# Kernel tuning notes

Measured on AMD Instinct MI355X. Metric: run time of the kernel, lower is better.

## Reference

```python
import jax, jax.numpy as jnp
import numpy as np

N = 100000   # nodes
E = 1600000  # edges
IN = 64
HID = 64
C = 2
EPS = 1e-12


def _linear_init(k, fan_in, fan_out):
    s = 1.0 / np.sqrt(fan_in)
    kw, kb = jax.random.split(k)
    w = jax.random.uniform(kw, (fan_in, fan_out), minval=-s, maxval=s, dtype=jnp.float32)
    b = jax.random.uniform(kb, (fan_out,), minval=-s, maxval=s, dtype=jnp.float32)
    return w, b


def setup_inputs() -> dict:
    key = jax.random.key(0)
    ks = jax.random.split(key, 12)
    x = jax.random.normal(ks[0], (N, IN), dtype=jnp.float32)
    edge_index = jax.random.randint(ks[1], (2, E), 0, N, dtype=jnp.int64)
    w1, b1 = _linear_init(ks[2], IN, HID)
    w2, b2 = _linear_init(ks[3], HID, HID)
    w3, b3 = _linear_init(ks[4], HID, HID)
    wg1, bg1 = _linear_init(ks[5], HID, HID)   # GCNConv 1
    wg2, bg2 = _linear_init(ks[6], HID, HID)   # GCNConv 2
    beta = jnp.ones((), dtype=jnp.float32)     # AGNN learnable scalar
    wf, bf = _linear_init(ks[7], HID, HID)     # W_f
    wx, bx = _linear_init(ks[8], HID, HID)     # W_x
    wc, bc = _linear_init(ks[9], 2 * HID, C)   # classifier
    return {"x": x, "edge_index": edge_index,
            "w1": w1, "b1": b1, "w2": w2, "b2": b2, "w3": w3, "b3": b3,
            "wg1": wg1, "bg1": bg1, "wg2": wg2, "bg2": bg2, "beta": beta,
            "wf": wf, "bf": bf, "wx": wx, "bx": bx, "wc": wc, "bc": bc}


def _segment_softmax(logits, seg, n):
    m = jax.ops.segment_max(logits, seg, num_segments=n)
    e = jnp.exp(logits - m[seg])
    s = jax.ops.segment_sum(e, seg, num_segments=n)
    return e / s[seg]


def _gcn_conv(x, w, b, row, col, norm):
    # x' = D^{-1/2}(A+I)D^{-1/2} x W + b  (PyG GCNConv with self-loops)
    h = x @ w                                   # [N, HID]
    msg = h[row] * norm[:, None]                # gather + scale  [E+N, HID]
    out = jax.ops.segment_sum(msg, col, num_segments=N)
    return out + b


def _agnn_conv(x, beta, row, col):
    # cosine-similarity attention (PyG AGNNConv), self-loops included
    xn = x / (jnp.linalg.norm(x, axis=-1, keepdims=True) + EPS)
    alpha = beta * jnp.sum(xn[row] * xn[col], axis=-1)   # [E+N]
    a = _segment_softmax(alpha, col, N)
    return jax.ops.segment_sum(a[:, None] * x[row], col, num_segments=N)


def reference(x, edge_index, w1, b1, w2, b2, w3, b3, wg1, bg1, wg2, bg2,
              beta, wf, bf, wx, bx, wc, bc):
    # add self-loops
    loop = jnp.arange(N, dtype=edge_index.dtype)
    row = jnp.concatenate([edge_index[0], loop])
    col = jnp.concatenate([edge_index[1], loop])
    # symmetric GCN normalization
    deg = jax.ops.segment_sum(jnp.ones_like(col, dtype=jnp.float32), col, num_segments=N)
    dinv = jnp.where(deg > 0, deg ** -0.5, 0.0)
    norm = dinv[row] * dinv[col]

    # input MLP
    h = jax.nn.relu(x @ w1 + b1)
    h = jax.nn.relu(h @ w2 + b2)
    h = h @ w3 + b3                              # [N, HID]

    f0 = _gcn_conv(h, wg1, bg1, row, col, norm)
    f1 = _gcn_conv(h, wg2, bg2, row, col, norm)
    h1 = _agnn_conv(h, beta, row, col)

    h_filters = jnp.stack([f0, f1], axis=1)      # [N, 2, HID]
    h_proj = jnp.tanh(h_filters @ wf + bf)       # [N, 2, HID]
    x_proj = jnp.tanh(h @ wx + bx)               # [N, HID]
    logit = jnp.einsum('nkh,nh->nk', h_proj, x_proj)   # bmm -> [N, 2]
    score = jax.nn.softmax(logit, axis=1)
    res = jnp.einsum('nkh,nk->nh', h_filters, score)   # attention-weighted fusion
    res = jnp.concatenate([res, h1], axis=1)     # [N, 2*HID]
    y_hat = res @ wc + bc                        # dropout disabled (eval)
    return y_hat
```

## Files before the change

### kernel.cpp

```cpp
#include <hip/hip_runtime.h>
#include <math.h>


#define SCT 8192

typedef float v2f __attribute__((ext_vector_type(2)));

__device__ __forceinline__ v2f v2fma(v2f a, v2f b, v2f c) {
#if __has_builtin(__builtin_elementwise_fma)
    return __builtin_elementwise_fma(a, b, c);
#else
    v2f r; r.x = fmaf(a.x, b.x, c.x); r.y = fmaf(a.y, b.y, c.y); return r;
#endif
}

__device__ __forceinline__ float fast_tanh(float x) {
    x = fminf(fmaxf(x, -15.f), 15.f);
    float e = __expf(2.f * x);
    return (e - 1.f) * __frcp_rn(e + 1.f);
}

__device__ __forceinline__ void fma4(float (&acc)[4], float a, const float4& w) {
    acc[0] = fmaf(a, w.x, acc[0]);
    acc[1] = fmaf(a, w.y, acc[1]);
    acc[2] = fmaf(a, w.z, acc[2]);
    acc[3] = fmaf(a, w.w, acc[3]);
}

__device__ __forceinline__ void load_rows32(const float* __restrict__ src, int row0, int n,
                                            float (*dst)[68], int t)
{
    int e = t * 8;
    int r = e >> 6, i = e & 63;
    int grow = row0 + r;
    float4 v0 = make_float4(0.f, 0.f, 0.f, 0.f), v1 = v0;
    if (grow < n) {
        const float* p = src + (size_t)grow * 64 + i;
        v0 = *(const float4*)p;
        v1 = *(const float4*)(p + 4);
    }
    *(float4*)&dst[r][i]     = v0;
    *(float4*)&dst[r][i + 4] = v1;
}

__device__ __forceinline__ void gemm_core(const float (*in)[68], const float* w,
                                          const float* b, int rg, int cg,
                                          float (&acc0)[4], float (&acc1)[4])
{
#pragma unroll
    for (int dc = 0; dc < 4; dc++) { float bb = b[4*cg + dc]; acc0[dc] = bb; acc1[dc] = bb; }
    const int r0 = 2 * rg, r1 = 2 * rg + 1;
#pragma unroll
    for (int i = 0; i < 64; i += 4) {
        float4 a0 = *(const float4*)&in[r0][i];
        float4 a1 = *(const float4*)&in[r1][i];
        float4 q0 = *(const float4*)&w[(i + 0) * 64 + 4 * cg];
        float4 q1 = *(const float4*)&w[(i + 1) * 64 + 4 * cg];
        float4 q2 = *(const float4*)&w[(i + 2) * 64 + 4 * cg];
        float4 q3 = *(const float4*)&w[(i + 3) * 64 + 4 * cg];
        fma4(acc0, a0.x, q0); fma4(acc0, a0.y, q1); fma4(acc0, a0.z, q2); fma4(acc0, a0.w, q3);
        fma4(acc1, a1.x, q0); fma4(acc1, a1.y, q1); fma4(acc1, a1.z, q2); fma4(acc1, a1.w, q3);
    }
}

__device__ __forceinline__ void gemm_core_gw(const float (*in)[68], const float* __restrict__ w,
                                             const float* b, int rg, int cg,
                                             float (&acc0)[4], float (&acc1)[4])
{
#pragma unroll
    for (int dc = 0; dc < 4; dc++) { float bb = b[4*cg + dc]; acc0[dc] = bb; acc1[dc] = bb; }
    const int r0 = 2 * rg, r1 = 2 * rg + 1;
    const float* wp = w + 4 * cg;
#pragma unroll 2
    for (int i = 0; i < 64; i += 4) {
        float4 a0 = *(const float4*)&in[r0][i];
        float4 a1 = *(const float4*)&in[r1][i];
        float4 q0 = *(const float4*)&wp[(size_t)(i + 0) * 64];
        float4 q1 = *(const float4*)&wp[(size_t)(i + 1) * 64];
        float4 q2 = *(const float4*)&wp[(size_t)(i + 2) * 64];
        float4 q3 = *(const float4*)&wp[(size_t)(i + 3) * 64];
        fma4(acc0, a0.x, q0); fma4(acc0, a0.y, q1); fma4(acc0, a0.z, q2); fma4(acc0, a0.w, q3);
        fma4(acc1, a1.x, q0); fma4(acc1, a1.y, q1); fma4(acc1, a1.z, q2); fma4(acc1, a1.w, q3);
    }
}

template <int MODE>
__device__ __forceinline__ void gemm_gw_lds(const float (*in)[68], const float* __restrict__ w,
                                            const float* b, float (*out)[68],
                                            int rg, int cg)
{
    float a0[4], a1[4];
    gemm_core_gw(in, w, b, rg, cg, a0, a1);
#pragma unroll
    for (int dc = 0; dc < 4; dc++) {
        float v0 = a0[dc], v1 = a1[dc];
        if (MODE == 1) { v0 = fmaxf(v0, 0.f); v1 = fmaxf(v1, 0.f); }
        a0[dc] = v0; a1[dc] = v1;
    }
    *(float4*)&out[2 * rg][4 * cg]     = make_float4(a0[0], a0[1], a0[2], a0[3]);
    *(float4*)&out[2 * rg + 1][4 * cg] = make_float4(a1[0], a1[1], a1[2], a1[3]);
}


__global__ __launch_bounds__(256) void k_zero(int* __restrict__ arr, int n1)
{
    int i = blockIdx.x * 256 + threadIdx.x;
    if (i < n1) arr[i] = 0;
}

__global__ __launch_bounds__(256) void k_bhist(const int* __restrict__ col,
                                               int* __restrict__ bhist, int e)
{
    __shared__ int hist[256];
    int t = threadIdx.x;
    hist[t] = 0;
    __syncthreads();
    int base = blockIdx.x * SCT;
    int end = min(e, base + SCT);
    for (int i = base + t; i < end; i += 256)
        atomicAdd(&hist[col[i] >> 9], 1);
    __syncthreads();
    if (hist[t]) atomicAdd(&bhist[t], hist[t]);
}

__global__ __launch_bounds__(256) void k_bscan(const int* __restrict__ bhist,
                                               int* __restrict__ bbase, int* __restrict__ bcur)
{
    __shared__ int s[256];
    int t = threadIdx.x;
    int v = bhist[t];
    s[t] = v;
    __syncthreads();
    for (int d = 1; d < 256; d <<= 1) {
        int u = (t >= d) ? s[t - d] : 0;
        __syncthreads();
        s[t] += u;
        __syncthreads();
    }
    int b = s[t] - v;
    bbase[t] = b;
    bcur[t] = b;
}

__global__ __launch_bounds__(256) void k_bscatter2(const int* __restrict__ row,
    const int* __restrict__ col, int* __restrict__ bcur,
    int2* __restrict__ pairs, int e, int nbk)
{
    __shared__ int hist[256], lcur[256], gb[256], s[256];
    __shared__ int2 buf[SCT];
    int t = threadIdx.x;
    int base = blockIdx.x * SCT;
    int end = min(e, base + SCT);
    hist[t] = 0;
    __syncthreads();
    for (int i = base + t; i < end; i += 256)
        atomicAdd(&hist[col[i] >> 9], 1);
    __syncthreads();
    int v = hist[t];
    s[t] = v;
    __syncthreads();
    for (int d = 1; d < 256; d <<= 1) {
        int u = (t >= d) ? s[t - d] : 0;
        __syncthreads();
        s[t] += u;
        __syncthreads();
    }
    lcur[t] = s[t] - v;
    __syncthreads();
    for (int i = base + t; i < end; i += 256) {
        int c = col[i];
        int slot = atomicAdd(&lcur[c >> 9], 1);
        buf[slot] = make_int2(row[i], c);
    }
    if (v > 0) gb[t] = atomicAdd(&bcur[t], v);
    __syncthreads();
    for (int b = 0; b < nbk; b++) {
        int cnt = hist[b];
        if (cnt == 0) continue;
        int lo = s[b] - cnt;
        int go = gb[b];
        for (int j = t; j < cnt; j += 256)
            pairs[go + j] = buf[lo + j];
    }
}

__global__ __launch_bounds__(256) void k_fill3(const int2* __restrict__ pairs,
    const int* __restrict__ bbase, const int* __restrict__ bhist,
    int* __restrict__ arr, int* __restrict__ csr, int n)
{
    __shared__ int nh[512], nc[512], s[256];
    int b = blockIdx.x, t = threadIdx.x;
    int pbase = bbase[b];
    int cnt = bhist[b];
    int nodebase = b << 9;
    nh[t] = 0; nh[t + 256] = 0;
    __syncthreads();
    for (int i = t; i < cnt; i += 256)
        atomicAdd(&nh[pairs[pbase + i].y - nodebase], 1);
    __syncthreads();
    int v0 = nh[2 * t], v1 = nh[2 * t + 1];
    int sum = v0 + v1;
    s[t] = sum;
    __syncthreads();
    for (int d = 1; d < 256; d <<= 1) {
        int u = (t >= d) ? s[t - d] : 0;
        __syncthreads();
        s[t] += u;
        __syncthreads();
    }
    int excl = s[t] - sum;
    int n0 = nodebase + 2 * t, n1 = n0 + 1;
    nc[2 * t]     = pbase + excl;
    nc[2 * t + 1] = pbase + excl + v0;
    if (n0 < n) arr[n0] = pbase + excl + v0;
    if (n1 < n) arr[n1] = pbase + excl + v0 + v1;
    __syncthreads();
    for (int i = t; i < cnt; i += 256) {
        int2 pr = pairs[pbase + i];
        int p = atomicAdd(&nc[pr.y - nodebase], 1);
        csr[p] = pr.x;
    }
}


__global__ __launch_bounds__(256) void k_pre(
    const float* __restrict__ wg1, const float* __restrict__ bg1,
    const float* __restrict__ wg2, const float* __restrict__ bg2,
    const float* __restrict__ wf,  const float* __restrict__ bf,
    const float* __restrict__ wc,  float* __restrict__ pre)
{
    __shared__ float wfs[4096];
    __shared__ float wcs[128];
    int t = threadIdx.x;
    for (int i = t; i < 4096; i += 256) wfs[i] = wf[i];
    if (t < 128) wcs[t] = wc[t];
    __syncthreads();
    int i = t & 63, jb = (t >> 6) * 16;
    float acc0[16], acc1[16];
#pragma unroll
    for (int j = 0; j < 16; j++) { acc0[j] = 0.f; acc1[j] = 0.f; }
#pragma unroll 1
    for (int k = 0; k < 64; k++) {
        float a = wg1[i * 64 + k];
        float b = wg2[i * 64 + k];
#pragma unroll
        for (int j = 0; j < 16; j++) {
            float w = wfs[k * 64 + jb + j];
            acc0[j] = fmaf(a, w, acc0[j]);
            acc1[j] = fmaf(b, w, acc1[j]);
        }
    }
#pragma unroll
    for (int j = 0; j < 16; j++) {
        pre[i * 64 + jb + j]        = acc0[j];
        pre[4096 + i * 64 + jb + j] = acc1[j];
    }
    if (t < 64) {
        float s0 = bf[t], s1 = bf[t];
#pragma unroll 1
        for (int m = 0; m < 64; m++) {
            s0 = fmaf(bg1[m], wfs[m * 64 + t], s0);
            s1 = fmaf(bg2[m], wfs[m * 64 + t], s1);
        }
        pre[8192 + t] = s0;
        pre[8256 + t] = s1;
        float u00 = 0.f, u01 = 0.f, u10 = 0.f, u11 = 0.f;
#pragma unroll 1
        for (int m = 0; m < 64; m++) {
            float g1 = wg1[t * 64 + m], g2 = wg2[t * 64 + m];
            u00 = fmaf(g1, wcs[m * 2 + 0], u00);
            u01 = fmaf(g1, wcs[m * 2 + 1], u01);
            u10 = fmaf(g2, wcs[m * 2 + 0], u10);
            u11 = fmaf(g2, wcs[m * 2 + 1], u11);
        }
        pre[8320 + t * 2]     = u00;
        pre[8320 + t * 2 + 1] = u01;
        pre[8448 + t * 2]     = u10;
        pre[8448 + t * 2 + 1] = u11;
    }
    if (t == 0) {
        float v00 = 0.f, v01 = 0.f, v10 = 0.f, v11 = 0.f;
#pragma unroll 1
        for (int m = 0; m < 64; m++) {
            v00 = fmaf(bg1[m], wcs[m * 2 + 0], v00);
            v01 = fmaf(bg1[m], wcs[m * 2 + 1], v01);
            v10 = fmaf(bg2[m], wcs[m * 2 + 0], v10);
            v11 = fmaf(bg2[m], wcs[m * 2 + 1], v11);
        }
        pre[8576] = v00; pre[8577] = v01; pre[8578] = v10; pre[8579] = v11;
    }
}


__global__ __launch_bounds__(256) void k_mlp(const float* __restrict__ x,
    const float* __restrict__ w1, const float* __restrict__ b1,
    const float* __restrict__ w2, const float* __restrict__ b2,
    const float* __restrict__ w3, const float* __restrict__ b3,
    const int* __restrict__ arr, float* __restrict__ h,
    float2* __restrict__ nrm2, int n)
{
    __shared__ float b1s[64], b2s[64], b3s[64];
    __shared__ float xs[32][68], hs[32][68];
    int t = threadIdx.x;
    if (t < 64) { b1s[t] = b1[t]; b2s[t] = b2[t]; b3s[t] = b3[t]; }
    __syncthreads();
    int cg = t & 15, rg = t >> 4;
    for (int row0 = blockIdx.x * 32; row0 < n; row0 += gridDim.x * 32) {
        load_rows32(x, row0, n, xs, t);
        __syncthreads();
        gemm_gw_lds<1>(xs, w1, b1s, hs, rg, cg);
        __syncthreads();
        gemm_gw_lds<1>(hs, w2, b2s, xs, rg, cg);
        __syncthreads();
        {
            float a0[4], a1[4];
            gemm_core_gw(xs, w3, b3s, rg, cg, a0, a1);
            int r0 = row0 + 2 * rg, r1 = r0 + 1;
            if (r0 < n) *(float4*)&h[(size_t)r0 * 64 + 4 * cg] = make_float4(a0[0], a0[1], a0[2], a0[3]);
            if (r1 < n) *(float4*)&h[(size_t)r1 * 64 + 4 * cg] = make_float4(a1[0], a1[1], a1[2], a1[3]);
            float s0 = a0[0]*a0[0] + a0[1]*a0[1] + a0[2]*a0[2] + a0[3]*a0[3];
            float s1 = a1[0]*a1[0] + a1[1]*a1[1] + a1[2]*a1[2] + a1[3]*a1[3];
#pragma unroll
            for (int d = 1; d < 16; d <<= 1) { s0 += __shfl_xor(s0, d, 64); s1 += __shfl_xor(s1, d, 64); }
            if (cg == 0) {
                if (r0 < n) {
                    int st = (r0 == 0) ? 0 : arr[r0 - 1];
                    nrm2[r0] = make_float2(1.0f / (sqrtf(s0) + 1e-12f),
                                           rsqrtf((float)(arr[r0] - st + 1)));
                }
                if (r1 < n) {
                    int st = arr[r1 - 1];
                    nrm2[r1] = make_float2(1.0f / (sqrtf(s1) + 1e-12f),
                                           rsqrtf((float)(arr[r1] - st + 1)));
                }
            }
        }
        __syncthreads();
    }
}


__global__ __launch_bounds__(256) void k_gather(const float* __restrict__ h,
    const int* __restrict__ arr, const int* __restrict__ csr,
    const float2* __restrict__ nrm2, const float* __restrict__ beta_p,
    const float* __restrict__ wc,
    float* __restrict__ agg, float2* __restrict__ yp, int n)
{
    __shared__ float reda[4][8][64];
    __shared__ float redn[4][8][64];
    int wv = threadIdx.x >> 6;
    int node = blockIdx.x * 4 + wv;
    if (node >= n) return;
    int lane = threadIdx.x & 63;
    int g = lane >> 3, s = lane & 7;
    float beta = beta_p[0];
    const char* hb = (const char*)h;

    unsigned selfoff = ((unsigned)node << 8) + ((unsigned)s << 5);
    float4 hA = *(const float4*)(hb + selfoff);
    float4 hB = *(const float4*)(hb + selfoff + 16);
    v2f hc0 = {hA.x, hA.y}, hc1 = {hA.z, hA.w};
    v2f hc2 = {hB.x, hB.y}, hc3 = {hB.z, hB.w};

    v2f sv = hc0 * hc0;
    sv = v2fma(hc1, hc1, sv); sv = v2fma(hc2, hc2, sv); sv = v2fma(hc3, hc3, sv);
    float ss = sv.x + sv.y;
#pragma unroll
    for (int d = 1; d < 8; d <<= 1) ss += __shfl_xor(ss, d, 64);
    float2 ncv = nrm2[node];
    float rnc = ncv.x, dc = ncv.y;
    float brn = beta * rnc;
    float wself = __expf(brn * ss * rnc);

    v2f a0 = {0.f,0.f}, a1 = {0.f,0.f}, a2 = {0.f,0.f}, a3 = {0.f,0.f};
    v2f n0 = {0.f,0.f}, n1 = {0.f,0.f}, n2 = {0.f,0.f}, n3 = {0.f,0.f};
    float denom = 0.f;
    if (g == 0) {
        v2f dcv = {dc, dc}, wsv = {wself, wself};
        a0 = dcv * hc0; a1 = dcv * hc1; a2 = dcv * hc2; a3 = dcv * hc3;
        n0 = wsv * hc0; n1 = wsv * hc1; n2 = wsv * hc2; n3 = wsv * hc3;
        denom = wself;
    }

    int start = (node == 0) ? 0 : arr[node - 1];
    int end = arr[node];
#pragma unroll 1
    for (int k0 = start; k0 < end; k0 += 64) {
        int m = min(64, end - k0);
        int idx = 0; float rv = 0.f, dv = 0.f;
        if (lane < m) {
            idx = csr[k0 + lane];
            float2 nd = nrm2[idx];
            rv = nd.x; dv = nd.y;
        }
        int ei = __shfl(idx, g, 64);
        unsigned eoff = ((unsigned)ei << 8) + ((unsigned)s << 5);
        float4 cA = *(const float4*)(hb + eoff);
        float4 cB = *(const float4*)(hb + eoff + 16);
#pragma unroll 1
        for (int k = 0; k < m; k += 8) {
            float4 fA = cA, fB = cB;
            if (k + 8 < m) {
                int e2 = __shfl(idx, k + 8 + g, 64);
                unsigned off2 = ((unsigned)e2 << 8) + ((unsigned)s << 5);
                cA = *(const float4*)(hb + off2);
                cB = *(const float4*)(hb + off2 + 16);
            }
            float rnr = __shfl(rv, k + g, 64);
            float dvr = __shfl(dv, k + g, 64);
            v2f f0 = {fA.x, fA.y}, f1 = {fA.z, fA.w};
            v2f f2 = {fB.x, fB.y}, f3 = {fB.z, fB.w};
            v2f ps = f0 * hc0;
            ps = v2fma(f1, hc1, ps); ps = v2fma(f2, hc2, ps); ps = v2fma(f3, hc3, ps);
            float p = ps.x + ps.y;
#pragma unroll
            for (int d = 1; d < 8; d <<= 1) p += __shfl_xor(p, d, 64);
            bool act = (k + g) < m;
            float w   = act ? __expf(brn * p * rnr) : 0.f;
            float dve = act ? dvr : 0.f;
            v2f wsp = {w, w}, dsp = {dve, dve};
            a0 = v2fma(dsp, f0, a0); a1 = v2fma(dsp, f1, a1);
            a2 = v2fma(dsp, f2, a2); a3 = v2fma(dsp, f3, a3);
            n0 = v2fma(wsp, f0, n0); n1 = v2fma(wsp, f1, n1);
            n2 = v2fma(wsp, f2, n2); n3 = v2fma(wsp, f3, n3);
            denom += w;
        }
    }

    {
        float* wa = &reda[wv][g][8 * s];
        float* wn = &redn[wv][g][8 * s];
        *(float4*)wa       = make_float4(a0.x, a0.y, a1.x, a1.y);
        *(float4*)(wa + 4) = make_float4(a2.x, a2.y, a3.x, a3.y);
        *(float4*)wn       = make_float4(n0.x, n0.y, n1.x, n1.y);
        *(float4*)(wn + 4) = make_float4(n2.x, n2.y, n3.x, n3.y);
    }
    const float* ra = &reda[wv][0][lane];
    const float* rn = &redn[wv][0][lane];
    float asum, nsum;
    {
        float t0 = ra[0]   + ra[64],  t1 = ra[128] + ra[192];
        float t2 = ra[256] + ra[320], t3 = ra[384] + ra[448];
        asum = (t0 + t1) + (t2 + t3);
        float u0 = rn[0]   + rn[64],  u1 = rn[128] + rn[192];
        float u2 = rn[256] + rn[320], u3 = rn[384] + rn[448];
        nsum = (u0 + u1) + (u2 + u3);
    }
    agg[(size_t)node * 64 + lane] = dc * asum;

#pragma unroll
    for (int d = 8; d < 64; d <<= 1) denom += __shfl_xor(denom, d, 64);

    float2 wcv = *(const float2*)(wc + 128 + 2 * lane);
    float cx = nsum * wcv.x, cy = nsum * wcv.y;
#pragma unroll
    for (int d = 1; d < 64; d <<= 1) { cx += __shfl_xor(cx, d, 64); cy += __shfl_xor(cy, d, 64); }
    if (lane == 0) {
        float inv = 1.0f / denom;
        yp[node] = make_float2(cx * inv, cy * inv);
    }
}


__global__ __launch_bounds__(256) void k_epi(const float* __restrict__ agg,
    const float* __restrict__ hbuf, const float2* __restrict__ yp,
    const float* __restrict__ pre, const float* __restrict__ wx,
    const float* __restrict__ bx, const float* __restrict__ bc,
    float* __restrict__ y, int n, int ntiles)
{
    __shared__ float W0s[4096], W1s[4096], wxs[4096];
    __shared__ float c0s[64], c1s[64], bxs[64], us[256], vs[4], bcs[2];
    __shared__ float A[32][68], H[32][68];
    int t = threadIdx.x;
    for (int i = t; i < 4096; i += 256) { W0s[i] = pre[i]; W1s[i] = pre[4096 + i]; wxs[i] = wx[i]; }
    if (t < 64) { c0s[t] = pre[8192 + t]; c1s[t] = pre[8256 + t]; bxs[t] = bx[t]; }
    us[t] = pre[8320 + t];
    if (t < 4) vs[t] = pre[8576 + t];
    if (t < 2) bcs[t] = bc[t];
    __syncthreads();
    int cg = t & 15, rg = t >> 4;
    for (int tile = blockIdx.x; tile < ntiles; tile += gridDim.x) {
        int row0 = tile * 32;
        load_rows32(agg,  row0, n, A, t);
        load_rows32(hbuf, row0, n, H, t);
        __syncthreads();
        int r0g = row0 + 2 * rg, r1g = r0g + 1;
        float xp0[4], xp1[4];
        gemm_core(H, wxs, bxs, rg, cg, xp0, xp1);
#pragma unroll
        for (int j = 0; j < 4; j++) { xp0[j] = fast_tanh(xp0[j]); xp1[j] = fast_tanh(xp1[j]); }
        float a0[4], a1[4];
        gemm_core(A, W0s, c0s, rg, cg, a0, a1);
        float l00 = 0.f, l01 = 0.f;
#pragma unroll
        for (int j = 0; j < 4; j++) {
            l00 = fmaf(fast_tanh(a0[j]), xp0[j], l00);
            l01 = fmaf(fast_tanh(a1[j]), xp1[j], l01);
        }
        gemm_core(A, W1s, c1s, rg, cg, a0, a1);
        float l10 = 0.f, l11 = 0.f;
#pragma unroll
        for (int j = 0; j < 4; j++) {
            l10 = fmaf(fast_tanh(a0[j]), xp0[j], l10);
            l11 = fmaf(fast_tanh(a1[j]), xp1[j], l11);
        }
        float4 av0 = *(const float4*)&A[2 * rg][4 * cg];
        float4 av1 = *(const float4*)&A[2 * rg + 1][4 * cg];
        float za0=0.f, za1=0.f, zb0=0.f, zb1=0.f;
        float zc0=0.f, zc1=0.f, zd0=0.f, zd1=0.f;
#pragma unroll
        for (int j = 0; j < 4; j++) {
            int k = 4 * cg + j;
            float u0c0 = us[k * 2], u0c1 = us[k * 2 + 1];
            float u1c0 = us[128 + k * 2], u1c1 = us[128 + k * 2 + 1];
            float p0 = (&av0.x)[j], p1 = (&av1.x)[j];
            za0 = fmaf(p0, u0c0, za0); za1 = fmaf(p0, u0c1, za1);
            zb0 = fmaf(p0, u1c0, zb0); zb1 = fmaf(p0, u1c1, zb1);
            zc0 = fmaf(p1, u0c0, zc0); zc1 = fmaf(p1, u0c1, zc1);
            zd0 = fmaf(p1, u1c0, zd0); zd1 = fmaf(p1, u1c1, zd1);
        }
#pragma unroll
        for (int d = 1; d < 16; d <<= 1) {
            l00 += __shfl_xor(l00, d, 64); l01 += __shfl_xor(l01, d, 64);
            l10 += __shfl_xor(l10, d, 64); l11 += __shfl_xor(l11, d, 64);
            za0 += __shfl_xor(za0, d, 64); za1 += __shfl_xor(za1, d, 64);
            zb0 += __shfl_xor(zb0, d, 64); zb1 += __shfl_xor(zb1, d, 64);
            zc0 += __shfl_xor(zc0, d, 64); zc1 += __shfl_xor(zc1, d, 64);
            zd0 += __shfl_xor(zd0, d, 64); zd1 += __shfl_xor(zd1, d, 64);
        }
        if (cg == 0) {
            if (r0g < n) {
                float mx = fmaxf(l00, l10);
                float e0 = __expf(l00 - mx), e1 = __expf(l10 - mx);
                float inv = 1.0f / (e0 + e1);
                float s0 = e0 * inv, s1 = e1 * inv;
                float2 ypv = yp[r0g];
                float y0v = s0 * (za0 + vs[0]) + s1 * (zb0 + vs[2]) + ypv.x + bcs[0];
                float y1v = s0 * (za1 + vs[1]) + s1 * (zb1 + vs[3]) + ypv.y + bcs[1];
                *(float2*)&y[(size_t)r0g * 2] = make_float2(y0v, y1v);
            }
            if (r1g < n) {
                float mx = fmaxf(l01, l11);
                float e0 = __expf(l01 - mx), e1 = __expf(l11 - mx);
                float inv = 1.0f / (e0 + e1);
                float s0 = e0 * inv, s1 = e1 * inv;
                float2 ypv = yp[r1g];
                float y0v = s0 * (zc0 + vs[0]) + s1 * (zd0 + vs[2]) + ypv.x + bcs[0];
                float y1v = s0 * (zc1 + vs[1]) + s1 * (zd1 + vs[3]) + ypv.y + bcs[1];
                *(float2*)&y[(size_t)r1g * 2] = make_float2(y0v, y1v);
            }
        }
        __syncthreads();
    }
}

extern "C" void kernel_launch(void* const* d_in, const int* in_sizes, int n_in,
                              void* d_out, int out_size, void* d_ws, size_t ws_size,
                              hipStream_t stream)
{
    const float* x    = (const float*)d_in[0];
    const int*   ei   = (const int*)d_in[1];
    const float* w1   = (const float*)d_in[2];
    const float* b1   = (const float*)d_in[3];
    const float* w2   = (const float*)d_in[4];
    const float* b2   = (const float*)d_in[5];
    const float* w3   = (const float*)d_in[6];
    const float* b3   = (const float*)d_in[7];
    const float* wg1  = (const float*)d_in[8];
    const float* bg1  = (const float*)d_in[9];
    const float* wg2  = (const float*)d_in[10];
    const float* bg2  = (const float*)d_in[11];
    const float* beta = (const float*)d_in[12];
    const float* wf   = (const float*)d_in[13];
    const float* bf   = (const float*)d_in[14];
    const float* wx   = (const float*)d_in[15];
    const float* bx   = (const float*)d_in[16];
    const float* wc   = (const float*)d_in[17];
    const float* bc   = (const float*)d_in[18];
    float* y = (float*)d_out;

    int n = in_sizes[0] / 64;
    int e = in_sizes[1] / 2;
    const int* row = ei;
    const int* col = ei + e;

    char* p = (char*)d_ws;
    auto alloc = [&](size_t bytes) { char* q = p; p += (bytes + 255) & ~(size_t)255; return q; };
    float*  h    = (float*)alloc((size_t)n * 64 * 4);
    int*    csr  = (int*)alloc((size_t)e * 4);
    float2* nrm2 = (float2*)alloc((size_t)n * 8);
    int*    arr  = (int*)alloc((size_t)(n + 1) * 4);
    float2* yp   = (float2*)alloc((size_t)n * 8);
    float*  pre  = (float*)alloc(8704 * 4);
    int*    bhist = (int*)alloc(256 * 4);
    int*    bbase = (int*)alloc(256 * 4);
    int*    bcur  = (int*)alloc(256 * 4);

    int2* pairs = (int2*)h;
    float* agg = (float*)d_in[0];

    int ntiles = (n + 31) / 32;
    int nbk = (n + 511) >> 9;
    int nsct = (e + SCT - 1) / SCT;

    k_pre<<<1, 256, 0, stream>>>(wg1, bg1, wg2, bg2, wf, bf, wc, pre);
    k_zero<<<1, 256, 0, stream>>>(bhist, 256);
    k_bhist<<<nsct, 256, 0, stream>>>(col, bhist, e);
    k_bscan<<<1, 256, 0, stream>>>(bhist, bbase, bcur);
    k_bscatter2<<<nsct, 256, 0, stream>>>(row, col, bcur, pairs, e, nbk);
    k_fill3<<<nbk, 256, 0, stream>>>(pairs, bbase, bhist, arr, csr, n);
    k_mlp<<<ntiles, 256, 0, stream>>>(x, w1, b1, w2, b2, w3, b3, arr, h, nrm2, n);
    k_gather<<<(n + 3) / 4, 256, 0, stream>>>(h, arr, csr, nrm2, beta, wc, agg, yp, n);
    k_epi<<<1024, 256, 0, stream>>>(agg, h, yp, pre, wx, bx, bc, y, n, ntiles);
}
```

Measured before the change: 428.3 us.

## Make MLP per-wave with 4 rows per thread and no block barriers

The input MLP kernel now gives each wavefront a private 16-row LDS tile. Each thread computes 4 rows by 4 columns, so every global weight load is reused across four rows instead of two. The block-wide __syncthreads are replaced with wave-local LDS waitcnt fences, and blocks now cover 64 rows. This is meant to halve weight-fetch traffic per output and remove block barrier stalls. The cost is more accumulator registers, and correctness relies on the wave executing in lockstep over its own LDS region.

```diff
diff --git a/kernel.cpp b/kernel.cpp
--- a/kernel.cpp
+++ b/kernel.cpp
@@ -12,6 +12,10 @@
 #else
     v2f r; r.x = fmaf(a.x, b.x, c.x); r.y = fmaf(a.y, b.y, c.y); return r;
 #endif
+}
+
+__device__ __forceinline__ void lds_fence() {
+    asm volatile("s_waitcnt lgkmcnt(0)" ::: "memory");
 }
 
 __device__ __forceinline__ float fast_tanh(float x) {
@@ -63,42 +67,30 @@
     }
 }
 
-__device__ __forceinline__ void gemm_core_gw(const float (*in)[68], const float* __restrict__ w,
-                                             const float* b, int rg, int cg,
-                                             float (&acc0)[4], float (&acc1)[4])
-{
-#pragma unroll
-    for (int dc = 0; dc < 4; dc++) { float bb = b[4*cg + dc]; acc0[dc] = bb; acc1[dc] = bb; }
-    const int r0 = 2 * rg, r1 = 2 * rg + 1;
+__device__ __forceinline__ void gemm4_gw(const float (*in)[68], const float* __restrict__ w,
+                                         const float* b, int rgs, int cg,
+                                         float (&acc)[4][4])
+{
+#pragma unroll
+    for (int r = 0; r < 4; r++) {
+#pragma unroll
+        for (int dc = 0; dc < 4; dc++) acc[r][dc] = b[4 * cg + dc];
+    }
     const float* wp = w + 4 * cg;
+    const int r0 = 4 * rgs;
 #pragma unroll 2
     for (int i = 0; i < 64; i += 4) {
-        float4 a0 = *(const float4*)&in[r0][i];
-        float4 a1 = *(const float4*)&in[r1][i];
-        float4 q0 = *(const float4*)&wp[(size_t)(i + 0) * 64];
-        float4 q1 = *(const float4*)&wp[(size_t)(i + 1) * 64];
-        float4 q2 = *(const float4*)&wp[(size_t)(i + 2) * 64];
-        float4 q3 = *(const float4*)&wp[(size_t)(i + 3) * 64];
-        fma4(acc0, a0.x, q0); fma4(acc0, a0.y, q1); fma4(acc0, a0.z, q2); fma4(acc0, a0.w, q3);
-        fma4(acc1, a1.x, q0); fma4(acc1, a1.y, q1); fma4(acc1, a1.z, q2); fma4(acc1, a1.w, q3);
-    }
-}
-
-template <int MODE>
-__device__ __forceinline__ void gemm_gw_lds(const float (*in)[68], const float* __restrict__ w,
-                                            const float* b, float (*out)[68],
-                                            int rg, int cg)
-{
-    float a0[4], a1[4];
-    gemm_core_gw(in, w, b, rg, cg, a0, a1);
-#pragma unroll
-    for (int dc = 0; dc < 4; dc++) {
-        float v0 = a0[dc], v1 = a1[dc];
-        if (MODE == 1) { v0 = fmaxf(v0, 0.f); v1 = fmaxf(v1, 0.f); }
-        a0[dc] = v0; a1[dc] = v1;
-    }
-    *(float4*)&out[2 * rg][4 * cg]     = make_float4(a0[0], a0[1], a0[2], a0[3]);
-    *(float4*)&out[2 * rg + 1][4 * cg] = make_float4(a1[0], a1[1], a1[2], a1[3]);
+        float4 q0 = *(const float4*)&wp[(i + 0) * 64];
+        float4 q1 = *(const float4*)&wp[(i + 1) * 64];
+        float4 q2 = *(const float4*)&wp[(i + 2) * 64];
+        float4 q3 = *(const float4*)&wp[(i + 3) * 64];
+#pragma unroll
+        for (int r = 0; r < 4; r++) {
+            float4 a = *(const float4*)&in[r0 + r][i];
+            fma4(acc[r], a.x, q0); fma4(acc[r], a.y, q1);
+            fma4(acc[r], a.z, q2); fma4(acc[r], a.w, q3);
+        }
+    }
 }
 
 
@@ -300,42 +292,74 @@
     float2* __restrict__ nrm2, int n)
 {
     __shared__ float b1s[64], b2s[64], b3s[64];
-    __shared__ float xs[32][68], hs[32][68];
+    __shared__ float xs[4][16][68];
     int t = threadIdx.x;
     if (t < 64) { b1s[t] = b1[t]; b2s[t] = b2[t]; b3s[t] = b3[t]; }
     __syncthreads();
-    int cg = t & 15, rg = t >> 4;
-    for (int row0 = blockIdx.x * 32; row0 < n; row0 += gridDim.x * 32) {
-        load_rows32(x, row0, n, xs, t);
-        __syncthreads();
-        gemm_gw_lds<1>(xs, w1, b1s, hs, rg, cg);
-        __syncthreads();
-        gemm_gw_lds<1>(hs, w2, b2s, xs, rg, cg);
-        __syncthreads();
-        {
-            float a0[4], a1[4];
-            gemm_core_gw(xs, w3, b3s, rg, cg, a0, a1);
-            int r0 = row0 + 2 * rg, r1 = r0 + 1;
-            if (r0 < n) *(float4*)&h[(size_t)r0 * 64 + 4 * cg] = make_float4(a0[0], a0[1], a0[2], a0[3]);
-            if (r1 < n) *(float4*)&h[(size_t)r1 * 64 + 4 * cg] = make_float4(a1[0], a1[1], a1[2], a1[3]);
-            float s0 = a0[0]*a0[0] + a0[1]*a0[1] + a0[2]*a0[2] + a0[3]*a0[3];
-            float s1 = a1[0]*a1[0] + a1[1]*a1[1] + a1[2]*a1[2] + a1[3]*a1[3];
-#pragma unroll
-            for (int d = 1; d < 16; d <<= 1) { s0 += __shfl_xor(s0, d, 64); s1 += __shfl_xor(s1, d, 64); }
-            if (cg == 0) {
-                if (r0 < n) {
-                    int st = (r0 == 0) ? 0 : arr[r0 - 1];
-                    nrm2[r0] = make_float2(1.0f / (sqrtf(s0) + 1e-12f),
-                                           rsqrtf((float)(arr[r0] - st + 1)));
-                }
-                if (r1 < n) {
-                    int st = arr[r1 - 1];
-                    nrm2[r1] = make_float2(1.0f / (sqrtf(s1) + 1e-12f),
-                                           rsqrtf((float)(arr[r1] - st + 1)));
-                }
+    int wv = t >> 6, lane = t & 63;
+    int cg = lane & 15, rgs = lane >> 4;
+    int row0 = blockIdx.x * 64 + wv * 16;
+    float (*ws)[68] = xs[wv];
+
+    {
+        int r = lane >> 2, c = (lane & 3) * 16;
+        int grow = row0 + r;
+        float4 v0 = make_float4(0.f,0.f,0.f,0.f), v1 = v0, v2 = v0, v3 = v0;
+        if (grow < n) {
+            const float* p = x + (size_t)grow * 64 + c;
+            v0 = *(const float4*)p;       v1 = *(const float4*)(p + 4);
+            v2 = *(const float4*)(p + 8); v3 = *(const float4*)(p + 12);
+        }
+        *(float4*)&ws[r][c]      = v0; *(float4*)&ws[r][c + 4]  = v1;
+        *(float4*)&ws[r][c + 8]  = v2; *(float4*)&ws[r][c + 12] = v3;
+    }
+    lds_fence();
+
+    float acc[4][4];
+    gemm4_gw(ws, w1, b1s, rgs, cg, acc);
+    lds_fence();
+#pragma unroll
+    for (int r = 0; r < 4; r++)
+        *(float4*)&ws[4 * rgs + r][4 * cg] =
+            make_float4(fmaxf(acc[r][0], 0.f), fmaxf(acc[r][1], 0.f),
+                        fmaxf(acc[r][2], 0.f), fmaxf(acc[r][3], 0.f));
+    lds_fence();
+    gemm4_gw(ws, w2, b2s, rgs, cg, acc);
+    lds_fence();
+#pragma unroll
+    for (int r = 0; r < 4; r++)
+        *(float4*)&ws[4 * rgs + r][4 * cg] =
+            make_float4(fmaxf(acc[r][0], 0.f), fmaxf(acc[r][1], 0.f),
+                        fmaxf(acc[r][2], 0.f), fmaxf(acc[r][3], 0.f));
+    lds_fence();
+    gemm4_gw(ws, w3, b3s, rgs, cg, acc);
+
+    int r0g = row0 + 4 * rgs;
+    float sr[4];
+#pragma unroll
+    for (int r = 0; r < 4; r++) {
+        int grow = r0g + r;
+        if (grow < n)
+            *(float4*)&h[(size_t)grow * 64 + 4 * cg] =
+                make_float4(acc[r][0], acc[r][1], acc[r][2], acc[r][3]);
+        sr[r] = acc[r][0]*acc[r][0] + acc[r][1]*acc[r][1]
+              + acc[r][2]*acc[r][2] + acc[r][3]*acc[r][3];
+    }
+#pragma unroll
+    for (int d = 1; d < 16; d <<= 1) {
+#pragma unroll
+        for (int r = 0; r < 4; r++) sr[r] += __shfl_xor(sr[r], d, 64);
+    }
+    if (cg == 0) {
+#pragma unroll
+        for (int r = 0; r < 4; r++) {
+            int grow = r0g + r;
+            if (grow < n) {
+                int st = (grow == 0) ? 0 : arr[grow - 1];
+                nrm2[grow] = make_float2(1.0f / (sqrtf(sr[r]) + 1e-12f),
+                                         rsqrtf((float)(arr[grow] - st + 1)));
             }
         }
-        __syncthreads();
     }
 }
 
@@ -600,6 +624,7 @@
     float* agg = (float*)d_in[0];
 
     int ntiles = (n + 31) / 32;
+    int ntile64 = (n + 63) / 64;
     int nbk = (n + 511) >> 9;
     int nsct = (e + SCT - 1) / SCT;
 
@@ -609,7 +634,7 @@
     k_bscan<<<1, 256, 0, stream>>>(bhist, bbase, bcur);
     k_bscatter2<<<nsct, 256, 0, stream>>>(row, col, bcur, pairs, e, nbk);
     k_fill3<<<nbk, 256, 0, stream>>>(pairs, bbase, bhist, arr, csr, n);
-    k_mlp<<<ntiles, 256, 0, stream>>>(x, w1, b1, w2, b2, w3, b3, arr, h, nrm2, n);
+    k_mlp<<<ntile64, 256, 0, stream>>>(x, w1, b1, w2, b2, w3, b3, arr, h, nrm2, n);
     k_gather<<<(n + 3) / 4, 256, 0, stream>>>(h, arr, csr, nrm2, beta, wc, agg, yp, n);
     k_epi<<<1024, 256, 0, stream>>>(agg, h, yp, pre, wx, bx, bc, y, n, ntiles);
 }
```

After: 401.4 us. -6.3%, faster.
